# Kernel tuning notes

Hardware: AMD Instinct MI355X
Metric: run time of the kernel (lower is better)

## Reference

```python
import jax, jax.numpy as jnp
import numpy as np

B, N, M = 256, 2207, 16          # graphs per batch, nodes per graph, mid_channel
E = 16777216                      # total edges in the batched graph
C1, C2 = 12, 4                    # global_conv1_dim, global_conv2_dim
H1, H2 = 256, 64                  # FC hidden sizes
EPS = 1e-5                        # LayerNorm / BatchNorm eps
BN_SCALE = 1.0 / np.sqrt(1.0 + EPS)  # eval BatchNorm with running_mean=0, running_var=1


def setup_inputs() -> dict:
    ks = jax.random.split(jax.random.key(0), 16)
    def nrm(i, shape, s):
        return jax.random.normal(ks[i], shape, jnp.float32) * s
    return {
        "x": jax.random.normal(ks[0], (B * N, 1), jnp.float32),
        "edge_index": jax.random.randint(ks[1], (2, E), 0, B * N, dtype=jnp.int32),
        "edge_weight": jax.random.uniform(ks[2], (E,), jnp.float32),
        # GraphConv: lin_rel (with bias) on aggregated neighbors + lin_root on self
        "w_root": nrm(3, (1, M), 0.5),
        "w_rel": nrm(4, (1, M), 0.5),
        "b_rel": jnp.full((M,), 0.01, jnp.float32),
        # LayerNorm over (num_nodes, mid_channel)
        "ln_g": jnp.ones((N, M), jnp.float32),
        "ln_b": jnp.zeros((N, M), jnp.float32),
        # 1x1 conv stacks
        "gc1_w": nrm(5, (C1, M), 0.3), "gc1_b": nrm(6, (C1,), 0.1),
        "bn1_g": jnp.ones((C1,), jnp.float32), "bn1_b": jnp.zeros((C1,), jnp.float32),
        "gc2_w": nrm(7, (C2, C1), 0.3), "gc2_b": nrm(8, (C2,), 0.1),
        "bn2_g": jnp.ones((C2,), jnp.float32), "bn2_b": jnp.zeros((C2,), jnp.float32),
        # FC stack (weights stored [in, out])
        "fc_w1": nrm(9, (C2 * N, H1), 0.02), "fc_b1": jnp.full((H1,), 0.01, jnp.float32),
        "fbn1_g": jnp.ones((H1,), jnp.float32), "fbn1_b": jnp.zeros((H1,), jnp.float32),
        "fc_w2": nrm(10, (H1, H2), 0.1), "fc_b2": jnp.full((H2,), 0.01, jnp.float32),
        "fbn2_g": jnp.ones((H2,), jnp.float32), "fbn2_b": jnp.zeros((H2,), jnp.float32),
        "fc1_w": nrm(11, (H2, 1), 0.1), "fc1_b": jnp.full((1,), 0.01, jnp.float32),
    }


def reference(x, edge_index, edge_weight, w_root, w_rel, b_rel, ln_g, ln_b,
              gc1_w, gc1_b, bn1_g, bn1_b, gc2_w, gc2_b, bn2_g, bn2_b,
              fc_w1, fc_b1, fbn1_g, fbn1_b, fc_w2, fc_b2, fbn2_g, fbn2_b,
              fc1_w, fc1_b):
    src, dst = edge_index[0], edge_index[1]
    # GraphConv: gather source features, weight, scatter-add to destinations
    agg = jax.ops.segment_sum(x[src] * edge_weight[:, None], dst, num_segments=B * N)
    h = jax.nn.relu(agg @ w_rel + b_rel + x @ w_root)          # [B*N, M]
    h = h.reshape(B, N, M)
    # LayerNorm over (N, M) per sample (biased variance, as in torch)
    mu = h.mean(axis=(1, 2), keepdims=True)
    var = ((h - mu) ** 2).mean(axis=(1, 2), keepdims=True)
    h = (h - mu) * jax.lax.rsqrt(var + EPS) * ln_g + ln_b
    h = h.transpose(0, 2, 1)                                   # [B, M, N]
    # 1x1 conv -> relu -> eval-BN (rm=0, rv=1)
    y = jax.nn.relu(jnp.einsum('oc,bcn->bon', gc1_w, h) + gc1_b[None, :, None])
    y = y * (BN_SCALE * bn1_g)[None, :, None] + bn1_b[None, :, None]
    y = jax.nn.relu(jnp.einsum('oc,bcn->bon', gc2_w, y) + gc2_b[None, :, None])
    y = y * (BN_SCALE * bn2_g)[None, :, None] + bn2_b[None, :, None]
    z = y.reshape(B, C2 * N)                                   # channel-major flatten, matches torch view
    z = z @ fc_w1 + fc_b1
    z = jax.nn.relu(z * (BN_SCALE * fbn1_g) + fbn1_b)
    z = z @ fc_w2 + fc_b2
    z = jax.nn.relu(z * (BN_SCALE * fbn2_g) + fbn2_b)
    return z @ fc1_w + fc1_b                                   # [B, 1]
```

## Files before the change

### kernel.cpp

```cpp
#include <hip/hip_runtime.h>
#include <hip/hip_bf16.h>

#define BB   256
#define NN   2207
#define MM   16
#define EE   16777216
#define CC1  12
#define CC2  4
#define HH1  256
#define HH2  64
#define KK1  (CC2*NN)
#define LN_EPS 1e-5f
#define BN_SCALE 0.9999950000374997f
#define NBK  256
#define MAGIC 1946067ull
#define EPB  4096
#define TPB  512
#define EPT  (EPB/TPB)
#define NBLK (EE/EPB)
#define GRP  4
#define NGRP (NBK/GRP)
#define RSP6 16

static __device__ __forceinline__ unsigned bucket_of(int d) {
    return (unsigned)(((unsigned long long)(unsigned)d * MAGIC) >> 32);
}

__global__ __launch_bounds__(TPB, 8)
void k_place4(const int* __restrict__ src, const int* __restrict__ dst,
              const float* __restrict__ ew,
              uint2* __restrict__ recs, unsigned short* __restrict__ stab)
{
    __shared__ unsigned int hist[NBK], start[NBK];
    __shared__ unsigned int wtot[4];

    const int t = threadIdx.x;
    if (t < NBK) hist[t] = 0;
    __syncthreads();

    const int i4base = blockIdx.x * (EPB/4);
    unsigned key[EPT];
    float    wv[EPT];
    unsigned short rk[EPT];
    unsigned char  bk[EPT];
    #pragma unroll
    for (int q = 0; q < EPT/4; ++q) {
        int i4 = i4base + q*TPB + t;
        int4   s4 = reinterpret_cast<const int4*>(src)[i4];
        int4   d4 = reinterpret_cast<const int4*>(dst)[i4];
        float4 w4 = reinterpret_cast<const float4*>(ew)[i4];
        unsigned b0 = bucket_of(d4.x), b1 = bucket_of(d4.y);
        unsigned b2 = bucket_of(d4.z), b3 = bucket_of(d4.w);
        unsigned r0 = atomicAdd(&hist[b0], 1u);
        unsigned r1 = atomicAdd(&hist[b1], 1u);
        unsigned r2 = atomicAdd(&hist[b2], 1u);
        unsigned r3 = atomicAdd(&hist[b3], 1u);
        key[q*4+0] = ((unsigned)s4.x << 12) | (unsigned)(d4.x - (int)(b0*NN));
        key[q*4+1] = ((unsigned)s4.y << 12) | (unsigned)(d4.y - (int)(b1*NN));
        key[q*4+2] = ((unsigned)s4.z << 12) | (unsigned)(d4.z - (int)(b2*NN));
        key[q*4+3] = ((unsigned)s4.w << 12) | (unsigned)(d4.w - (int)(b3*NN));
        wv[q*4+0] = w4.x; wv[q*4+1] = w4.y; wv[q*4+2] = w4.z; wv[q*4+3] = w4.w;
        rk[q*4+0] = (unsigned short)r0; rk[q*4+1] = (unsigned short)r1;
        rk[q*4+2] = (unsigned short)r2; rk[q*4+3] = (unsigned short)r3;
        bk[q*4+0] = (unsigned char)b0; bk[q*4+1] = (unsigned char)b1;
        bk[q*4+2] = (unsigned char)b2; bk[q*4+3] = (unsigned char)b3;
    }
    __syncthreads();

    if (t < NBK) {
        unsigned h = hist[t], v = h;
        #pragma unroll
        for (int off = 1; off < 64; off <<= 1) {
            unsigned u = __shfl_up(v, off);
            if ((t & 63) >= off) v += u;
        }
        start[t] = v - h;
        if ((t & 63) == 63) wtot[t >> 6] = v;
    }
    __syncthreads();
    if (t < NBK) {
        const int w = t >> 6;
        unsigned wo = 0;
        if (w > 0) wo += wtot[0];
        if (w > 1) wo += wtot[1];
        if (w > 2) wo += wtot[2];
        start[t] += wo;
        stab[blockIdx.x * NBK + t] = (unsigned short)(start[t]);
    }
    __syncthreads();

    uint2* rb = recs + (size_t)blockIdx.x * EPB;
    #pragma unroll
    for (int e = 0; e < EPT; ++e)
        rb[start[bk[e]] + (unsigned)rk[e]] =
            make_uint2(key[e], __float_as_uint(wv[e]));
}

__global__ __launch_bounds__(512, 8)
void k_replay6(const uint2* __restrict__ recs, const unsigned short* __restrict__ stab,
               const float* __restrict__ x, float* __restrict__ paggr)
{
    __shared__ float acc[GRP*NN];
    const int t = threadIdx.x;
    const int g = blockIdx.x & (NGRP - 1);
    const int r = blockIdx.x >> 6;
    for (int n = t; n < GRP*NN; n += 512) acc[n] = 0.f;
    __syncthreads();

    const int lane = t & 63, w = t >> 6;
    const int nreg = NBLK / RSP6;
    const int reg0 = r * nreg;
    const int j0 = g * GRP;

    int region = reg0 + w;
    const unsigned short* sb = stab + (size_t)region * NBK + j0;
    unsigned c0 = sb[0], c1 = sb[1], c2 = sb[2], c3 = sb[3];
    unsigned c4 = (j0 + GRP < NBK) ? (unsigned)sb[4] : (unsigned)EPB;

    for (int ri = w; ri < nreg; ri += 8) {
        const unsigned b0 = c0, b1 = c1, b2 = c2, b3 = c3, b4 = c4;
        const uint2* rp = recs + (size_t)region * EPB;
        const int regionN = region + 8;
        if (ri + 8 < nreg) {
            const unsigned short* sbn = stab + (size_t)regionN * NBK + j0;
            c0 = sbn[0]; c1 = sbn[1]; c2 = sbn[2]; c3 = sbn[3];
            c4 = (j0 + GRP < NBK) ? (unsigned)sbn[4] : (unsigned)EPB;
        }
        for (unsigned u = b0 + (unsigned)lane; u < b4; u += 64u) {
            uint2 rec = rp[u];
            unsigned so = (u >= b1) + (u >= b2) + (u >= b3);
            atomicAdd(&acc[so * NN + (rec.x & 0xFFFu)],
                      x[rec.x >> 12] * __uint_as_float(rec.y));
        }
        region = regionN;
    }
    __syncthreads();
    float* pa = paggr + (((size_t)r * NGRP + g) * GRP) * NN;
    for (int n = t; n < GRP*NN; n += 512) pa[n] = acc[n];
}

__global__ __launch_bounds__(512)
void k_ln_conv(const float* __restrict__ x, const float* __restrict__ paggr,
              const float* __restrict__ w_root, const float* __restrict__ w_rel,
              const float* __restrict__ b_rel,
              const float* __restrict__ ln_g, const float* __restrict__ ln_b,
              const float* __restrict__ gc1_w, const float* __restrict__ gc1_b,
              const float* __restrict__ bn1_g, const float* __restrict__ bn1_b,
              const float* __restrict__ gc2_w, const float* __restrict__ gc2_b,
              const float* __restrict__ bn2_g, const float* __restrict__ bn2_b,
              float* __restrict__ z)
{
    __shared__ float xs[NN], acc[NN];
    __shared__ float gw1[CC1*MM], gb1[CC1], sb1[CC1], tb1[CC1];
    __shared__ float gw2[CC2*CC1], gb2[CC2], sb2[CC2], tb2[CC2];
    __shared__ float redS[8], redQ[8];
    __shared__ float s_mu, s_rs;

    const int b = blockIdx.x, t = threadIdx.x;
    const float* xb = x + b*NN;
    const float* pb = paggr + (((size_t)(b >> 2)) * GRP + (b & 3)) * NN;
    const size_t rstride = (size_t)NGRP * GRP * NN;
    for (int n = t; n < NN; n += 512) {
        xs[n] = xb[n];
        float a = 0.f;
        #pragma unroll
        for (int r = 0; r < RSP6; ++r)
            a += pb[(size_t)r * rstride + n];
        acc[n] = a;
    }
    if (t < CC1*MM) gw1[t] = gc1_w[t];
    if (t >= 192 && t < 192+CC1) { int o = t-192; gb1[o]=gc1_b[o]; sb1[o]=BN_SCALE*bn1_g[o]; tb1[o]=bn1_b[o]; }
    if (t >= 208 && t < 208+CC2*CC1) gw2[t-208] = gc2_w[t-208];
    if (t >= 240 && t < 240+CC2) { int p=t-240; gb2[p]=gc2_b[p]; sb2[p]=BN_SCALE*bn2_g[p]; tb2[p]=bn2_b[p]; }

    float wr[MM], br[MM], wo[MM];
    #pragma unroll
    for (int m = 0; m < MM; ++m) { wr[m]=w_rel[m]; br[m]=b_rel[m]; wo[m]=w_root[m]; }
    __syncthreads();

    float S = 0.f, Q = 0.f;
    for (int n = t; n < NN; n += 512) {
        float a = acc[n], xv = xs[n];
        #pragma unroll
        for (int m = 0; m < MM; ++m) {
            float h = fmaxf(fmaf(a, wr[m], fmaf(xv, wo[m], br[m])), 0.f);
            S += h; Q += h*h;
        }
    }
    #pragma unroll
    for (int off = 32; off; off >>= 1) { S += __shfl_down(S, off); Q += __shfl_down(Q, off); }
    if ((t & 63) == 0) { redS[t>>6] = S; redQ[t>>6] = Q; }
    __syncthreads();
    if (t == 0) {
        float SS = 0.f, QQ = 0.f;
        #pragma unroll
        for (int i = 0; i < 8; ++i) { SS += redS[i]; QQ += redQ[i]; }
        const float inv = 1.f / (float)(NN*MM);
        float mu = SS * inv;
        float var = QQ * inv - mu*mu;
        s_mu = mu; s_rs = rsqrtf(var + LN_EPS);
    }
    __syncthreads();
    const float mu = s_mu, rs = s_rs;

    float* zb = z + (size_t)b * KK1;
    for (int n = t; n < NN; n += 512) {
        float a = acc[n], xv = xs[n];
        float hn[MM];
        const float4* g4  = reinterpret_cast<const float4*>(ln_g + n*MM);
        const float4* be4 = reinterpret_cast<const float4*>(ln_b + n*MM);
        #pragma unroll
        for (int q = 0; q < 4; ++q) {
            float4 g = g4[q], be = be4[q];
            float gg[4]  = {g.x, g.y, g.z, g.w};
            float bb_[4] = {be.x, be.y, be.z, be.w};
            #pragma unroll
            for (int j = 0; j < 4; ++j) {
                int m = q*4 + j;
                float h = fmaxf(fmaf(a, wr[m], fmaf(xv, wo[m], br[m])), 0.f);
                hn[m] = (h - mu) * rs * gg[j] + bb_[j];
            }
        }
        float y1[CC1];
        #pragma unroll
        for (int o = 0; o < CC1; ++o) {
            float a1 = gb1[o];
            #pragma unroll
            for (int m = 0; m < MM; ++m) a1 = fmaf(gw1[o*MM+m], hn[m], a1);
            y1[o] = fmaxf(a1, 0.f) * sb1[o] + tb1[o];
        }
        #pragma unroll
        for (int p = 0; p < CC2; ++p) {
            float a2 = gb2[p];
            #pragma unroll
            for (int o = 0; o < CC1; ++o) a2 = fmaf(gw2[p*CC1+o], y1[o], a2);
            zb[p*NN + n] = fmaxf(a2, 0.f) * sb2[p] + tb2[p];
        }
    }
}

#define GK_CHUNK 288
__global__ __launch_bounds__(256)
void k_fc1_part(const float* __restrict__ z, const float* __restrict__ W1,
                float* __restrict__ out1_part)
{
    __shared__ float zs[64*36];
    __shared__ float ws_[32*68];
    const int bt = blockIdx.x, jt = blockIdx.y, ks = blockIdx.z;
    const int t = threadIdx.x;
    const int tb = t >> 4, tj = t & 15;
    const int k0 = ks * GK_CHUNK;
    const int kend = min(k0 + GK_CHUNK, KK1);
    float acc[4][4] = {};
    const int zrow = t >> 2, zcol = (t & 3) * 8;
    const int wrow = t >> 3, wcol = (t & 7) * 8;

    for (int kc = k0; kc < kend; kc += 32) {
        const float* zsrc = z + (size_t)(bt*64 + zrow)*KK1 + kc + zcol;
        #pragma unroll
        for (int q = 0; q < 2; ++q) {
            int k = kc + zcol + q*4;
            float4 v;
            if (k + 3 < kend) v = *reinterpret_cast<const float4*>(zsrc + q*4);
            else {
                v.x = (k+0 < kend) ? zsrc[q*4+0] : 0.f;
                v.y = (k+1 < kend) ? zsrc[q*4+1] : 0.f;
                v.z = (k+2 < kend) ? zsrc[q*4+2] : 0.f;
                v.w = (k+3 < kend) ? zsrc[q*4+3] : 0.f;
            }
            *reinterpret_cast<float4*>(&zs[zrow*36 + zcol + q*4]) = v;
        }
        {
            int k = kc + wrow;
            const float* wsrc = W1 + (size_t)k*HH1 + jt*64 + wcol;
            #pragma unroll
            for (int q = 0; q < 2; ++q) {
                float4 v;
                if (k < kend) v = *reinterpret_cast<const float4*>(wsrc + q*4);
                else v = float4{0.f,0.f,0.f,0.f};
                *reinterpret_cast<float4*>(&ws_[wrow*68 + wcol + q*4]) = v;
            }
        }
        __syncthreads();
        #pragma unroll
        for (int kk = 0; kk < 32; ++kk) {
            float4 w4 = *reinterpret_cast<const float4*>(&ws_[kk*68 + tj*4]);
            float zv[4], wv[4] = {w4.x, w4.y, w4.z, w4.w};
            #pragma unroll
            for (int ib = 0; ib < 4; ++ib) zv[ib] = zs[(tb*4+ib)*36 + kk];
            #pragma unroll
            for (int ib = 0; ib < 4; ++ib)
                #pragma unroll
                for (int ij = 0; ij < 4; ++ij)
                    acc[ib][ij] = fmaf(zv[ib], wv[ij], acc[ib][ij]);
        }
        __syncthreads();
    }
    #pragma unroll
    for (int ib = 0; ib < 4; ++ib) {
        int row = bt*64 + tb*4 + ib;
        float4 v = make_float4(acc[ib][0], acc[ib][1], acc[ib][2], acc[ib][3]);
        *reinterpret_cast<float4*>(
            &out1_part[((size_t)ks*256 + row)*HH1 + jt*64 + tj*4]) = v;
    }
}

__global__ __launch_bounds__(256)
void k_tail_part(const float* __restrict__ out1_part,
            const float* __restrict__ fc_b1, const float* __restrict__ fbn1_g,
            const float* __restrict__ fbn1_b,
            const float* __restrict__ W2, const float* __restrict__ fc_b2,
            const float* __restrict__ fbn2_g, const float* __restrict__ fbn2_b,
            const float* __restrict__ fc1_w, const float* __restrict__ fc1_b,
            float* __restrict__ out)
{
    __shared__ float o1s[HH1];
    const int b = blockIdx.x, t = threadIdx.x;
    float raw = fc_b1[t];
    #pragma unroll 4
    for (int ks = 0; ks < 31; ++ks)
        raw += out1_part[((size_t)ks*256 + b)*HH1 + t];
    o1s[t] = fmaxf(raw * (BN_SCALE * fbn1_g[t]) + fbn1_b[t], 0.f);
    __syncthreads();
    if (t < HH2) {
        float acc = fc_b2[t];
        #pragma unroll 4
        for (int j = 0; j < HH1; ++j) acc = fmaf(o1s[j], W2[j*HH2 + t], acc);
        float v2 = fmaxf(acc * (BN_SCALE * fbn2_g[t]) + fbn2_b[t], 0.f);
        float c = v2 * fc1_w[t];
        #pragma unroll
        for (int off = 32; off; off >>= 1) c += __shfl_down(c, off);
        if (t == 0) out[b] = c + fc1_b[0];
    }
}

__global__ __launch_bounds__(256)
void k_edge(const int* __restrict__ src, const int* __restrict__ dst,
            const float* __restrict__ ew, const float* __restrict__ x,
            float* __restrict__ agg)
{
    int i = blockIdx.x * 256 + threadIdx.x;
    const int4   s4 = reinterpret_cast<const int4*>(src)[i];
    const int4   d4 = reinterpret_cast<const int4*>(dst)[i];
    const float4 w4 = reinterpret_cast<const float4*>(ew)[i];
    unsafeAtomicAdd(&agg[d4.x], x[s4.x] * w4.x);
    unsafeAtomicAdd(&agg[d4.y], x[s4.y] * w4.y);
    unsafeAtomicAdd(&agg[d4.z], x[s4.z] * w4.z);
    unsafeAtomicAdd(&agg[d4.w], x[s4.w] * w4.w);
}

__global__ __launch_bounds__(256)
void k_sample(const float* __restrict__ x, const float* __restrict__ agg,
              const float* __restrict__ w_root, const float* __restrict__ w_rel,
              const float* __restrict__ b_rel,
              const float* __restrict__ ln_g, const float* __restrict__ ln_b,
              const float* __restrict__ gc1_w, const float* __restrict__ gc1_b,
              const float* __restrict__ bn1_g, const float* __restrict__ bn1_b,
              const float* __restrict__ gc2_w, const float* __restrict__ gc2_b,
              const float* __restrict__ bn2_g, const float* __restrict__ bn2_b,
              float* __restrict__ z)
{
    __shared__ float xs[NN], as[NN];
    __shared__ float gw1[CC1*MM], gb1[CC1], sb1[CC1], tb1[CC1];
    __shared__ float gw2[CC2*CC1], gb2[CC2], sb2[CC2], tb2[CC2];
    __shared__ float redS[4], redQ[4];
    __shared__ float s_mu, s_rs;

    const int b = blockIdx.x, t = threadIdx.x;
    const float* xb = x + b*NN;
    const float* ab = agg + b*NN;
    for (int n = t; n < NN; n += 256) { xs[n] = xb[n]; as[n] = ab[n]; }
    if (t < CC1*MM) gw1[t] = gc1_w[t];
    if (t >= 192 && t < 192+CC1) { int o = t-192; gb1[o]=gc1_b[o]; sb1[o]=BN_SCALE*bn1_g[o]; tb1[o]=bn1_b[o]; }
    if (t >= 208 && t < 208+CC2*CC1) gw2[t-208] = gc2_w[t-208];
    if (t >= 240 && t < 240+CC2) { int p=t-240; gb2[p]=gc2_b[p]; sb2[p]=BN_SCALE*bn2_g[p]; tb2[p]=bn2_b[p]; }

    float wr[MM], br[MM], wo[MM];
    #pragma unroll
    for (int m = 0; m < MM; ++m) { wr[m]=w_rel[m]; br[m]=b_rel[m]; wo[m]=w_root[m]; }
    __syncthreads();

    float S = 0.f, Q = 0.f;
    for (int n = t; n < NN; n += 256) {
        float a = as[n], xv = xs[n];
        #pragma unroll
        for (int m = 0; m < MM; ++m) {
            float h = fmaxf(fmaf(a, wr[m], fmaf(xv, wo[m], br[m])), 0.f);
            S += h; Q += h*h;
        }
    }
    #pragma unroll
    for (int off = 32; off; off >>= 1) { S += __shfl_down(S, off); Q += __shfl_down(Q, off); }
    if ((t & 63) == 0) { redS[t>>6] = S; redQ[t>>6] = Q; }
    __syncthreads();
    if (t == 0) {
        float SS = redS[0]+redS[1]+redS[2]+redS[3];
        float QQ = redQ[0]+redQ[1]+redQ[2]+redQ[3];
        const float inv = 1.f / (float)(NN*MM);
        float mu = SS * inv;
        float var = QQ * inv - mu*mu;
        s_mu = mu; s_rs = rsqrtf(var + LN_EPS);
    }
    __syncthreads();
    const float mu = s_mu, rs = s_rs;

    float* zb = z + (size_t)b * KK1;
    for (int n = t; n < NN; n += 256) {
        float a = as[n], xv = xs[n];
        float hn[MM];
        const float4* g4  = reinterpret_cast<const float4*>(ln_g + n*MM);
        const float4* be4 = reinterpret_cast<const float4*>(ln_b + n*MM);
        #pragma unroll
        for (int q = 0; q < 4; ++q) {
            float4 g = g4[q], be = be4[q];
            float gg[4]  = {g.x, g.y, g.z, g.w};
            float bb_[4] = {be.x, be.y, be.z, be.w};
            #pragma unroll
            for (int j = 0; j < 4; ++j) {
                int m = q*4 + j;
                float h = fmaxf(fmaf(a, wr[m], fmaf(xv, wo[m], br[m])), 0.f);
                hn[m] = (h - mu) * rs * gg[j] + bb_[j];
            }
        }
        float y1[CC1];
        #pragma unroll
        for (int o = 0; o < CC1; ++o) {
            float a1 = gb1[o];
            #pragma unroll
            for (int m = 0; m < MM; ++m) a1 = fmaf(gw1[o*MM+m], hn[m], a1);
            y1[o] = fmaxf(a1, 0.f) * sb1[o] + tb1[o];
        }
        #pragma unroll
        for (int p = 0; p < CC2; ++p) {
            float a2 = gb2[p];
            #pragma unroll
            for (int o = 0; o < CC1; ++o) a2 = fmaf(gw2[p*CC1+o], y1[o], a2);
            zb[p*NN + n] = fmaxf(a2, 0.f) * sb2[p] + tb2[p];
        }
    }
}

__global__ __launch_bounds__(256)
void k_fc1(const float* __restrict__ z, const float* __restrict__ W1,
           float* __restrict__ out1_raw)
{
    __shared__ float zs[64*36];
    __shared__ float ws_[32*68];
    const int bt = blockIdx.x, jt = blockIdx.y, ks = blockIdx.z;
    const int t = threadIdx.x;
    const int tb = t >> 4, tj = t & 15;
    const int k0 = ks * GK_CHUNK;
    const int kend = min(k0 + GK_CHUNK, KK1);
    float acc[4][4] = {};
    const int zrow = t >> 2, zcol = (t & 3) * 8;
    const int wrow = t >> 3, wcol = (t & 7) * 8;

    for (int kc = k0; kc < kend; kc += 32) {
        const float* zsrc = z + (size_t)(bt*64 + zrow)*KK1 + kc + zcol;
        #pragma unroll
        for (int q = 0; q < 2; ++q) {
            int k = kc + zcol + q*4;
            float4 v;
            if (k + 3 < kend) v = *reinterpret_cast<const float4*>(zsrc + q*4);
            else {
                v.x = (k+0 < kend) ? zsrc[q*4+0] : 0.f;
                v.y = (k+1 < kend) ? zsrc[q*4+1] : 0.f;
                v.z = (k+2 < kend) ? zsrc[q*4+2] : 0.f;
                v.w = (k+3 < kend) ? zsrc[q*4+3] : 0.f;
            }
            *reinterpret_cast<float4*>(&zs[zrow*36 + zcol + q*4]) = v;
        }
        {
            int k = kc + wrow;
            const float* wsrc = W1 + (size_t)k*HH1 + jt*64 + wcol;
            #pragma unroll
            for (int q = 0; q < 2; ++q) {
                float4 v;
                if (k < kend) v = *reinterpret_cast<const float4*>(wsrc + q*4);
                else v = float4{0.f,0.f,0.f,0.f};
                *reinterpret_cast<float4*>(&ws_[wrow*68 + wcol + q*4]) = v;
            }
        }
        __syncthreads();
        #pragma unroll
        for (int kk = 0; kk < 32; ++kk) {
            float4 w4 = *reinterpret_cast<const float4*>(&ws_[kk*68 + tj*4]);
            float zv[4], wv[4] = {w4.x, w4.y, w4.z, w4.w};
            #pragma unroll
            for (int ib = 0; ib < 4; ++ib) zv[ib] = zs[(tb*4+ib)*36 + kk];
            #pragma unroll
            for (int ib = 0; ib < 4; ++ib)
                #pragma unroll
                for (int ij = 0; ij < 4; ++ij)
                    acc[ib][ij] = fmaf(zv[ib], wv[ij], acc[ib][ij]);
        }
        __syncthreads();
    }
    #pragma unroll
    for (int ib = 0; ib < 4; ++ib) {
        int row = bt*64 + tb*4 + ib;
        #pragma unroll
        for (int ij = 0; ij < 4; ++ij)
            unsafeAtomicAdd(&out1_raw[row*HH1 + jt*64 + tj*4 + ij], acc[ib][ij]);
    }
}

__global__ __launch_bounds__(256)
void k_tail(const float* __restrict__ out1_raw,
            const float* __restrict__ fc_b1, const float* __restrict__ fbn1_g,
            const float* __restrict__ fbn1_b,
            const float* __restrict__ W2, const float* __restrict__ fc_b2,
            const float* __restrict__ fbn2_g, const float* __restrict__ fbn2_b,
            const float* __restrict__ fc1_w, const float* __restrict__ fc1_b,
            float* __restrict__ out)
{
    __shared__ float o1s[HH1];
    const int b = blockIdx.x, t = threadIdx.x;
    float raw = out1_raw[b*HH1 + t] + fc_b1[t];
    o1s[t] = fmaxf(raw * (BN_SCALE * fbn1_g[t]) + fbn1_b[t], 0.f);
    __syncthreads();
    if (t < HH2) {
        float acc = fc_b2[t];
        #pragma unroll 4
        for (int j = 0; j < HH1; ++j) acc = fmaf(o1s[j], W2[j*HH2 + t], acc);
        float v2 = fmaxf(acc * (BN_SCALE * fbn2_g[t]) + fbn2_b[t], 0.f);
        float c = v2 * fc1_w[t];
        #pragma unroll
        for (int off = 32; off; off >>= 1) c += __shfl_down(c, off);
        if (t == 0) out[b] = c + fc1_b[0];
    }
}

extern "C" void kernel_launch(void* const* d_in, const int* in_sizes, int n_in,
                              void* d_out, int out_size, void* d_ws, size_t ws_size,
                              hipStream_t stream)
{
    const float* x      = (const float*)d_in[0];
    const int*   ei     = (const int*)  d_in[1];
    const float* ew     = (const float*)d_in[2];
    const float* w_root = (const float*)d_in[3];
    const float* w_rel  = (const float*)d_in[4];
    const float* b_rel  = (const float*)d_in[5];
    const float* ln_g   = (const float*)d_in[6];
    const float* ln_b   = (const float*)d_in[7];
    const float* gc1_w  = (const float*)d_in[8];
    const float* gc1_b  = (const float*)d_in[9];
    const float* bn1_g  = (const float*)d_in[10];
    const float* bn1_b  = (const float*)d_in[11];
    const float* gc2_w  = (const float*)d_in[12];
    const float* gc2_b  = (const float*)d_in[13];
    const float* bn2_g  = (const float*)d_in[14];
    const float* bn2_b  = (const float*)d_in[15];
    const float* fc_w1  = (const float*)d_in[16];
    const float* fc_b1  = (const float*)d_in[17];
    const float* fbn1_g = (const float*)d_in[18];
    const float* fbn1_b = (const float*)d_in[19];
    const float* fc_w2  = (const float*)d_in[20];
    const float* fc_b2  = (const float*)d_in[21];
    const float* fbn2_g = (const float*)d_in[22];
    const float* fbn2_b = (const float*)d_in[23];
    const float* fc1_w  = (const float*)d_in[24];
    const float* fc1_b  = (const float*)d_in[25];
    float* out = (float*)d_out;

    char* ws = (char*)d_ws;
    const size_t off_recs  = 0;
    const size_t off_stab  = off_recs + (size_t)NBLK*EPB*8;
    const size_t off_paggr = off_stab + (size_t)NBLK*NBK*2;
    const size_t sz_paggr  = (size_t)RSP6*NGRP*GRP*NN*4;
    const size_t off_zbuf  = off_paggr + sz_paggr;
    const size_t need      = off_zbuf + (size_t)BB*KK1*4;

    if (ws_size >= need) {
        uint2*          recs  = (uint2*)(ws + off_recs);
        unsigned short* stab  = (unsigned short*)(ws + off_stab);
        float*          paggr = (float*)(ws + off_paggr);
        float*          zbuf  = (float*)(ws + off_zbuf);
        float*          o1p   = (float*)(ws + off_paggr);

        k_place4<<<NBLK, TPB, 0, stream>>>(ei, ei + EE, ew, recs, stab);
        k_replay6<<<NGRP*RSP6, 512, 0, stream>>>(recs, stab, x, paggr);
        k_ln_conv<<<BB, 512, 0, stream>>>(x, paggr,
                                         w_root, w_rel, b_rel, ln_g, ln_b,
                                         gc1_w, gc1_b, bn1_g, bn1_b,
                                         gc2_w, gc2_b, bn2_g, bn2_b, zbuf);
        k_fc1_part<<<dim3(4,4,31), 256, 0, stream>>>(zbuf, fc_w1, o1p);
        k_tail_part<<<BB, 256, 0, stream>>>(o1p, fc_b1, fbn1_g, fbn1_b,
                                       fc_w2, fc_b2, fbn2_g, fbn2_b,
                                       fc1_w, fc1_b, out);
    } else {
        float* agg      = (float*)(ws);
        float* zbuf     = (float*)(ws + 2259968);
        float* out1_raw = (float*)(ws + 2259968 + 9039872);

        hipMemsetAsync(agg,      0, (size_t)BB*NN*sizeof(float),  stream);
        hipMemsetAsync(out1_raw, 0, (size_t)BB*HH1*sizeof(float), stream);

        k_edge<<<EE/4/256, 256, 0, stream>>>(ei, ei + EE, ew, x, agg);
        k_sample<<<BB, 256, 0, stream>>>(x, agg, w_root, w_rel, b_rel, ln_g, ln_b,
                                         gc1_w, gc1_b, bn1_g, bn1_b,
                                         gc2_w, gc2_b, bn2_g, bn2_b, zbuf);
        k_fc1<<<dim3(4,4,31), 256, 0, stream>>>(zbuf, fc_w1, out1_raw);
        k_tail<<<BB, 256, 0, stream>>>(out1_raw, fc_b1, fbn1_g, fbn1_b,
                                       fc_w2, fc_b2, fbn2_g, fbn2_b,
                                       fc1_w, fc1_b, out);
    }
}
```

Baseline: 308.4 us.

## Gather x in placement pass and bucket edges by 4-graph group

The placement kernel now gathers x[src] and multiplies it by the edge weight up front, storing the product with a group-local destination index. Buckets are coarsened to 64 groups of four graphs, so the prefix scan fits in one wavefront and the replay kernel loops over one contiguous range without per-record sub-bucket tests or x gathers. This moves the random x gather into the streaming placement pass, where it can overlap with the coalesced loads. It also shrinks the offset table and simplifies replay. The record size stays the same, and the random gathers now happen in the placement kernel instead.

```diff
diff --git a/kernel.cpp b/kernel.cpp
--- a/kernel.cpp
+++ b/kernel.cpp
@@ -19,28 +19,27 @@
 #define EPT  (EPB/TPB)
 #define NBLK (EE/EPB)
 #define GRP  4
-#define NGRP (NBK/GRP)
-#define RSP6 16
+#define NBG  (NBK/GRP)
+#define RSPL 16
+#define GNN  (GRP*NN)
 
 static __device__ __forceinline__ unsigned bucket_of(int d) {
     return (unsigned)(((unsigned long long)(unsigned)d * MAGIC) >> 32);
 }
 
 __global__ __launch_bounds__(TPB, 8)
-void k_place4(const int* __restrict__ src, const int* __restrict__ dst,
-              const float* __restrict__ ew,
+void k_place5(const int* __restrict__ src, const int* __restrict__ dst,
+              const float* __restrict__ ew, const float* __restrict__ x,
               uint2* __restrict__ recs, unsigned short* __restrict__ stab)
 {
-    __shared__ unsigned int hist[NBK], start[NBK];
-    __shared__ unsigned int wtot[4];
-
+    __shared__ unsigned int hist[NBG], start[NBG];
     const int t = threadIdx.x;
-    if (t < NBK) hist[t] = 0;
+    if (t < NBG) hist[t] = 0;
     __syncthreads();
 
     const int i4base = blockIdx.x * (EPB/4);
-    unsigned key[EPT];
-    float    wv[EPT];
+    unsigned short key[EPT];
+    float          vv[EPT];
     unsigned short rk[EPT];
     unsigned char  bk[EPT];
     #pragma unroll
@@ -49,43 +48,36 @@
         int4   s4 = reinterpret_cast<const int4*>(src)[i4];
         int4   d4 = reinterpret_cast<const int4*>(dst)[i4];
         float4 w4 = reinterpret_cast<const float4*>(ew)[i4];
-        unsigned b0 = bucket_of(d4.x), b1 = bucket_of(d4.y);
-        unsigned b2 = bucket_of(d4.z), b3 = bucket_of(d4.w);
-        unsigned r0 = atomicAdd(&hist[b0], 1u);
-        unsigned r1 = atomicAdd(&hist[b1], 1u);
-        unsigned r2 = atomicAdd(&hist[b2], 1u);
-        unsigned r3 = atomicAdd(&hist[b3], 1u);
-        key[q*4+0] = ((unsigned)s4.x << 12) | (unsigned)(d4.x - (int)(b0*NN));
-        key[q*4+1] = ((unsigned)s4.y << 12) | (unsigned)(d4.y - (int)(b1*NN));
-        key[q*4+2] = ((unsigned)s4.z << 12) | (unsigned)(d4.z - (int)(b2*NN));
-        key[q*4+3] = ((unsigned)s4.w << 12) | (unsigned)(d4.w - (int)(b3*NN));
-        wv[q*4+0] = w4.x; wv[q*4+1] = w4.y; wv[q*4+2] = w4.z; wv[q*4+3] = w4.w;
+        float x0 = x[s4.x], x1 = x[s4.y], x2 = x[s4.z], x3 = x[s4.w];
+        unsigned sm0 = bucket_of(d4.x), sm1 = bucket_of(d4.y);
+        unsigned sm2 = bucket_of(d4.z), sm3 = bucket_of(d4.w);
+        unsigned g0 = sm0 >> 2, g1 = sm1 >> 2, g2 = sm2 >> 2, g3 = sm3 >> 2;
+        unsigned r0 = atomicAdd(&hist[g0], 1u);
+        unsigned r1 = atomicAdd(&hist[g1], 1u);
+        unsigned r2 = atomicAdd(&hist[g2], 1u);
+        unsigned r3 = atomicAdd(&hist[g3], 1u);
+        key[q*4+0] = (unsigned short)((unsigned)d4.x - (sm0 & ~3u) * NN);
+        key[q*4+1] = (unsigned short)((unsigned)d4.y - (sm1 & ~3u) * NN);
+        key[q*4+2] = (unsigned short)((unsigned)d4.z - (sm2 & ~3u) * NN);
+        key[q*4+3] = (unsigned short)((unsigned)d4.w - (sm3 & ~3u) * NN);
+        vv[q*4+0] = x0 * w4.x; vv[q*4+1] = x1 * w4.y;
+        vv[q*4+2] = x2 * w4.z; vv[q*4+3] = x3 * w4.w;
         rk[q*4+0] = (unsigned short)r0; rk[q*4+1] = (unsigned short)r1;
         rk[q*4+2] = (unsigned short)r2; rk[q*4+3] = (unsigned short)r3;
-        bk[q*4+0] = (unsigned char)b0; bk[q*4+1] = (unsigned char)b1;
-        bk[q*4+2] = (unsigned char)b2; bk[q*4+3] = (unsigned char)b3;
-    }
-    __syncthreads();
-
-    if (t < NBK) {
+        bk[q*4+0] = (unsigned char)g0; bk[q*4+1] = (unsigned char)g1;
+        bk[q*4+2] = (unsigned char)g2; bk[q*4+3] = (unsigned char)g3;
+    }
+    __syncthreads();
+
+    if (t < NBG) {
         unsigned h = hist[t], v = h;
         #pragma unroll
         for (int off = 1; off < 64; off <<= 1) {
             unsigned u = __shfl_up(v, off);
-            if ((t & 63) >= off) v += u;
+            if (t >= off) v += u;
         }
         start[t] = v - h;
-        if ((t & 63) == 63) wtot[t >> 6] = v;
-    }
-    __syncthreads();
-    if (t < NBK) {
-        const int w = t >> 6;
-        unsigned wo = 0;
-        if (w > 0) wo += wtot[0];
-        if (w > 1) wo += wtot[1];
-        if (w > 2) wo += wtot[2];
-        start[t] += wo;
-        stab[blockIdx.x * NBK + t] = (unsigned short)(start[t]);
+        stab[blockIdx.x * NBG + t] = (unsigned short)(v - h);
     }
     __syncthreads();
 
@@ -93,50 +85,45 @@
     #pragma unroll
     for (int e = 0; e < EPT; ++e)
         rb[start[bk[e]] + (unsigned)rk[e]] =
-            make_uint2(key[e], __float_as_uint(wv[e]));
+            make_uint2((unsigned)key[e], __float_as_uint(vv[e]));
 }
 
 __global__ __launch_bounds__(512, 8)
-void k_replay6(const uint2* __restrict__ recs, const unsigned short* __restrict__ stab,
-               const float* __restrict__ x, float* __restrict__ paggr)
-{
-    __shared__ float acc[GRP*NN];
+void k_replay7(const uint2* __restrict__ recs, const unsigned short* __restrict__ stab,
+               float* __restrict__ paggr)
+{
+    __shared__ float acc[GNN];
     const int t = threadIdx.x;
-    const int g = blockIdx.x & (NGRP - 1);
+    const int g = blockIdx.x & (NBG - 1);
     const int r = blockIdx.x >> 6;
-    for (int n = t; n < GRP*NN; n += 512) acc[n] = 0.f;
+    for (int n = t; n < GNN; n += 512) acc[n] = 0.f;
     __syncthreads();
 
     const int lane = t & 63, w = t >> 6;
-    const int nreg = NBLK / RSP6;
-    const int reg0 = r * nreg;
-    const int j0 = g * GRP;
-
-    int region = reg0 + w;
-    const unsigned short* sb = stab + (size_t)region * NBK + j0;
-    unsigned c0 = sb[0], c1 = sb[1], c2 = sb[2], c3 = sb[3];
-    unsigned c4 = (j0 + GRP < NBK) ? (unsigned)sb[4] : (unsigned)EPB;
-
+    const int nreg = NBLK / RSPL;
+    int region = r * nreg + w;
+
+    unsigned s0n = stab[(size_t)region * NBG + g];
+    unsigned s1n = (g < NBG-1) ? (unsigned)stab[(size_t)region * NBG + g + 1]
+                               : (unsigned)EPB;
     for (int ri = w; ri < nreg; ri += 8) {
-        const unsigned b0 = c0, b1 = c1, b2 = c2, b3 = c3, b4 = c4;
+        const unsigned b0 = s0n, b1 = s1n;
         const uint2* rp = recs + (size_t)region * EPB;
         const int regionN = region + 8;
         if (ri + 8 < nreg) {
-            const unsigned short* sbn = stab + (size_t)regionN * NBK + j0;
-            c0 = sbn[0]; c1 = sbn[1]; c2 = sbn[2]; c3 = sbn[3];
-            c4 = (j0 + GRP < NBK) ? (unsigned)sbn[4] : (unsigned)EPB;
-        }
-        for (unsigned u = b0 + (unsigned)lane; u < b4; u += 64u) {
+            s0n = stab[(size_t)regionN * NBG + g];
+            s1n = (g < NBG-1) ? (unsigned)stab[(size_t)regionN * NBG + g + 1]
+                              : (unsigned)EPB;
+        }
+        for (unsigned u = b0 + (unsigned)lane; u < b1; u += 64u) {
             uint2 rec = rp[u];
-            unsigned so = (u >= b1) + (u >= b2) + (u >= b3);
-            atomicAdd(&acc[so * NN + (rec.x & 0xFFFu)],
-                      x[rec.x >> 12] * __uint_as_float(rec.y));
+            atomicAdd(&acc[rec.x], __uint_as_float(rec.y));
         }
         region = regionN;
     }
     __syncthreads();
-    float* pa = paggr + (((size_t)r * NGRP + g) * GRP) * NN;
-    for (int n = t; n < GRP*NN; n += 512) pa[n] = acc[n];
+    float* pa = paggr + ((size_t)r * NBG + g) * GNN;
+    for (int n = t; n < GNN; n += 512) pa[n] = acc[n];
 }
 
 __global__ __launch_bounds__(512)
@@ -158,13 +145,13 @@
 
     const int b = blockIdx.x, t = threadIdx.x;
     const float* xb = x + b*NN;
-    const float* pb = paggr + (((size_t)(b >> 2)) * GRP + (b & 3)) * NN;
-    const size_t rstride = (size_t)NGRP * GRP * NN;
+    const float* pb = paggr + ((size_t)(b >> 2)) * GNN + (size_t)(b & 3) * NN;
+    const size_t rstride = (size_t)NBG * GNN;
     for (int n = t; n < NN; n += 512) {
         xs[n] = xb[n];
         float a = 0.f;
         #pragma unroll
-        for (int r = 0; r < RSP6; ++r)
+        for (int r = 0; r < RSPL; ++r)
             a += pb[(size_t)r * rstride + n];
         acc[n] = a;
     }
@@ -566,8 +553,8 @@
     char* ws = (char*)d_ws;
     const size_t off_recs  = 0;
     const size_t off_stab  = off_recs + (size_t)NBLK*EPB*8;
-    const size_t off_paggr = off_stab + (size_t)NBLK*NBK*2;
-    const size_t sz_paggr  = (size_t)RSP6*NGRP*GRP*NN*4;
+    const size_t off_paggr = off_stab + (size_t)NBLK*NBG*2;
+    const size_t sz_paggr  = (size_t)RSPL*NBG*GNN*4;
     const size_t off_zbuf  = off_paggr + sz_paggr;
     const size_t need      = off_zbuf + (size_t)BB*KK1*4;
 
@@ -578,8 +565,8 @@
         float*          zbuf  = (float*)(ws + off_zbuf);
         float*          o1p   = (float*)(ws + off_paggr);
 
-        k_place4<<<NBLK, TPB, 0, stream>>>(ei, ei + EE, ew, recs, stab);
-        k_replay6<<<NGRP*RSP6, 512, 0, stream>>>(recs, stab, x, paggr);
+        k_place5<<<NBLK, TPB, 0, stream>>>(ei, ei + EE, ew, x, recs, stab);
+        k_replay7<<<NBG*RSPL, 512, 0, stream>>>(recs, stab, paggr);
         k_ln_conv<<<BB, 512, 0, stream>>>(x, paggr,
                                          w_root, w_rel, b_rel, ln_g, ln_b,
                                          gc1_w, gc1_b, bn1_g, bn1_b,
```

Result: slower. 348.4 us (+13.0%).
